# Kernel optimization log

Measured on AMD Instinct MI355X. Metric: run time of the kernel, lower is better.

The kernel has to match this reference:

```python
import jax, jax.numpy as jnp
import numpy as np

N_AGENTS = 32
N_HEADS = 8
HEAD_DIM = 32          # atten_dim // n_heads
HID = 256              # rnn_hidden_dim
ATT = 256              # atten_dim
N_ACT = 32
NEG = -1e9             # finite stand-in for -inf; exp underflows to 0 in softmax


def setup_inputs() -> dict:
    key = jax.random.key(0)
    ks = jax.random.split(key, 20)
    B, N, E = 4096, 64, 128
    w = lambda k, shape: (jax.random.normal(k, shape, jnp.float32) * 0.05)
    return {
        "inputs": jax.random.normal(ks[0], (B, N, E), jnp.float32),
        "hidden_state": jax.random.normal(ks[1], (B, N_AGENTS, HID), jnp.float32) * 0.1,
        "fc1_w": w(ks[2], (HID, E)), "fc1_b": jnp.zeros((HID,), jnp.float32),
        "q_w": w(ks[3], (ATT, HID)), "q_b": jnp.zeros((ATT,), jnp.float32),
        "k_w": w(ks[4], (ATT, HID)), "k_b": jnp.zeros((ATT,), jnp.float32),
        "v_w": w(ks[5], (ATT, HID)), "v_b": jnp.zeros((ATT,), jnp.float32),
        "w_ih": w(ks[6], (3 * HID, ATT)), "w_hh": w(ks[7], (3 * HID, HID)),
        "b_ih": jnp.zeros((3 * HID,), jnp.float32), "b_hh": jnp.zeros((3 * HID,), jnp.float32),
        "out_w": w(ks[8], (N_ACT, HID)), "out_b": jnp.zeros((N_ACT,), jnp.float32),
        "obs_mask": jax.random.randint(ks[9], (B, N, N), 0, 2).astype(bool),
        "scenario_mask": jax.random.randint(ks[10], (B, N_AGENTS), 0, 2).astype(bool),
    }


def reference(inputs, hidden_state, fc1_w, fc1_b, q_w, q_b, k_w, k_b, v_w, v_b,
              w_ih, w_hh, b_ih, b_hh, out_w, out_b, obs_mask, scenario_mask):
    B, N, _ = inputs.shape
    A, nh, e = N_AGENTS, N_HEADS, HEAD_DIM
    # fc1 + ReLU: [B, N, HID]
    x = jax.nn.relu(inputs @ fc1_w.T + fc1_b)
    # multi-head projections; queries only for the first A entities (agents)
    q = (x[:, :A] @ q_w.T + q_b).reshape(B, A, nh, e).transpose(0, 2, 1, 3)   # [B,nh,A,e]
    k = (x @ k_w.T + k_b).reshape(B, N, nh, e).transpose(0, 2, 3, 1)          # [B,nh,e,N]
    v = jax.nn.relu(x @ v_w.T + v_b).reshape(B, N, nh, e).transpose(0, 2, 1, 3)  # [B,nh,N,e]
    score = jnp.einsum('bhae,bhen->bhan', q, k) / np.float32(np.sqrt(e))      # [B,nh,A,N]
    m = obs_mask[:, :A, :][:, None, :, :]                                      # [B,1,A,N]
    score = jnp.where(m, NEG, score)
    w = jax.nn.softmax(score, axis=-1)
    # original: fully-masked rows give NaN then are zeroed; here zero all masked slots
    w = jnp.where(m, 0.0, w)
    att = jnp.einsum('bhan,bhne->bhae', w, v)                                  # [B,nh,A,e]
    att = att.transpose(0, 2, 1, 3).reshape(B * A, nh * e)                     # [B*A, ATT]
    # GRUCell step (PyTorch gate ordering: r, z, n)
    h0 = hidden_state.reshape(B * A, HID)
    gi = att @ w_ih.T + b_ih
    gh = h0 @ w_hh.T + b_hh
    ir, iz, in_ = jnp.split(gi, 3, axis=-1)
    hr, hz, hn = jnp.split(gh, 3, axis=-1)
    r = jax.nn.sigmoid(ir + hr)
    z = jax.nn.sigmoid(iz + hz)
    n = jnp.tanh(in_ + r * hn)
    h = (1.0 - z) * n + z * h0
    h = h.reshape(B, A, HID)
    am = scenario_mask[:, :, None]                                             # [B,A,1]
    h = jnp.where(am, 0.0, h)
    q_out = h @ out_w.T + out_b
    q_out = jnp.where(am, 0.0, q_out)
    return q_out, h
```

## Files before the change

### kernel.cpp

```cpp
#include <hip/hip_runtime.h>


using bfrag = __attribute__((ext_vector_type(8))) short;
using ffrag = __attribute__((ext_vector_type(4))) float;

#define MFMA(a,b,c) __builtin_amdgcn_mfma_f32_16x16x32_bf16((a),(b),(c),0,0,0)
#define SWZ(row,col,S,xm) ((row)*(S) + ((((col)&~7) ^ (((row)&(xm))<<3)) | ((col)&7)))

#define OFF_A2   0L
#define OFF_FC1  67108864L
#define OFF_QKV  67141632L
#define OFF_W6   67338240L
#define OFF_OW   67731456L
#define OFF_FLAG 67739648L
#define WS_NEED_BYTES 135479552L

__device__ inline unsigned short f2bf(float x){
  union { float f; unsigned u; } v; v.f = x;
  unsigned r = v.u + 0x7fffu + ((v.u >> 16) & 1u);
  return (unsigned short)(r >> 16);
}
__device__ inline bool getmask(const void* p, long i, int byteflag){
  return byteflag ? (((const unsigned char*)p)[i] != 0)
                  : (((const int*)p)[i] != 0);
}
__device__ inline ffrag fzero(){ ffrag z; z[0]=0.f; z[1]=0.f; z[2]=0.f; z[3]=0.f; return z; }
__device__ inline void gload16(const short* g, short* l){
  __builtin_amdgcn_global_load_lds((const __attribute__((address_space(1))) void*)g,
                                   (__attribute__((address_space(3))) void*)l, 16, 0, 0);
}
__device__ inline bfrag packbf(const float* p){
  float4 f0 = *(const float4*)p; float4 f1 = *(const float4*)(p+4);
  bfrag v;
  v[0]=(short)f2bf(f0.x); v[1]=(short)f2bf(f0.y); v[2]=(short)f2bf(f0.z); v[3]=(short)f2bf(f0.w);
  v[4]=(short)f2bf(f1.x); v[5]=(short)f2bf(f1.y); v[6]=(short)f2bf(f1.z); v[7]=(short)f2bf(f1.w);
  return v;
}

__global__ void k0_prep(const float* __restrict__ fc1, const float* __restrict__ qw,
    const float* __restrict__ kw, const float* __restrict__ vw, const float* __restrict__ wih,
    const float* __restrict__ whh, const float* __restrict__ ow,
    const void* __restrict__ obsm, short* __restrict__ ws){
  long tid = (long)blockIdx.x*blockDim.x + threadIdx.x;
  long n = (long)gridDim.x*blockDim.x;
  if (tid == 0){
    const int* mi = (const int*)obsm;
    int f = 0;
    for (int i=0;i<256;i++){ if ((unsigned)mi[i] > 1u){ f = 1; break; } }
    ((int*)(ws + OFF_FLAG))[0] = f;
  }
  for (long i=tid; i<32768; i+=n){
    int R = (int)(i>>7), c = (int)(i&127);
    int seg = R>>6, r = R&63;
    ws[OFF_FC1 + ((long)(seg*64+r)<<7) + (c ^ ((r&7)<<3))] = (short)f2bf(fc1[i]);
  }
  for (long i=tid; i<65536; i+=n){
    int R = (int)(i>>8), C = (int)(i&255);
    int cb = R>>6, r = R&63, kh = C>>7, ck = C&127;
    int cs = ck ^ ((r&7)<<3);
    ws[OFF_QKV + ((long)(((0*4+cb)*2+kh)*64 + r)<<7) + cs] = (short)f2bf(qw[i]);
    ws[OFF_QKV + ((long)(((1*4+cb)*2+kh)*64 + r)<<7) + cs] = (short)f2bf(kw[i]);
    ws[OFF_QKV + ((long)(((2*4+cb)*2+kh)*64 + r)<<7) + cs] = (short)f2bf(vw[i]);
  }
  for (long i=tid; i<196608; i+=n){
    int gate = (int)(i >> 16);
    int grow = (int)((i >> 8) & 255);
    int c = (int)(i & 255);
    int jb = grow >> 5, row = grow & 31;
    int cs = c ^ ((row&7)<<3);
    ws[OFF_W6 + ((long)((jb*6 + gate)*32 + row))*256 + cs]     = (short)f2bf(wih[i]);
    ws[OFF_W6 + ((long)((jb*6 + 3 + gate)*32 + row))*256 + cs] = (short)f2bf(whh[i]);
  }
  for (long i=tid; i<8192; i+=n) ws[OFF_OW+i] = (short)f2bf(ow[i]);
}

__global__ __launch_bounds__(512) void k1_fused(const float* __restrict__ inp,
    const short* __restrict__ fc1S, const float* __restrict__ fc1_b,
    const short* __restrict__ qkvS,
    const float* __restrict__ qb, const float* __restrict__ kb, const float* __restrict__ vb,
    const void* __restrict__ obsm, short* __restrict__ A2, const int* __restrict__ flagp){
  __shared__ __align__(16) short smem[75776];
  short* x_s  = smem;
  short* wbuf = smem + 16384;
  short* p_sb = smem + 16384;
  short* a_s  = smem + 32768;
  short* q_s  = smem + 32768;
  short* k_s  = smem + 40960;
  short* vT_s = smem + 57344;
  unsigned char* m8 = (unsigned char*)(smem + 73728);
  int t = threadIdx.x; int b = blockIdx.x;
  int lane = t&63, w = t>>6, lr = lane&15, ko = lane>>4;
  int mflag = *flagp;
  auto STG = [&](const short* src, short* dst){
    #pragma unroll
    for (int i=0;i<2;i++)
      gload16(src + (long)(i*512 + t)*8, dst + (i*512 + (t&~63))*8);
  };
  STG(fc1S, wbuf);
  #pragma unroll
  for (int i=0;i<2;i++){
    int c = t + i*512; int row = c>>4; int cc = (c&15)*8;
    *(bfrag*)(a_s + SWZ(row, cc, 128, 7)) = packbf(inp + ((long)b*64 + row)*128 + cc);
  }
  if (mflag){
    uchar4 mv = *(const uchar4*)((const unsigned char*)obsm + (long)b*4096 + t*4);
    m8[t*4]=mv.x; m8[t*4+1]=mv.y; m8[t*4+2]=mv.z; m8[t*4+3]=mv.w;
  } else {
    int4 mv = *(const int4*)((const int*)obsm + (long)b*4096 + t*4);
    m8[t*4]  =(unsigned char)(mv.x!=0); m8[t*4+1]=(unsigned char)(mv.y!=0);
    m8[t*4+2]=(unsigned char)(mv.z!=0); m8[t*4+3]=(unsigned char)(mv.w!=0);
  }
  __syncthreads();
  {
    int rg1 = w&3, ch1 = w>>2;
    bfrag a1[4];
    #pragma unroll
    for (int ks=0;ks<4;ks++)
      a1[ks] = *(const bfrag*)(a_s + SWZ(rg1*16+lr, ks*32+ko*8, 128, 7));
    for (int s=0;s<4;s++){
      STG((s<3) ? (fc1S + (s+1)*8192) : qkvS, wbuf + ((s+1)&1)*8192);
      const short* wc = wbuf + (s&1)*8192;
      ffrag acc[2]; acc[0]=fzero(); acc[1]=fzero();
      #pragma unroll
      for (int ks=0;ks<4;ks++){
        int kc = ks*32+ko*8;
        #pragma unroll
        for (int nt=0;nt<2;nt++){
          bfrag bb = *(const bfrag*)(wc + SWZ(ch1*32+nt*16+lr, kc, 128, 7));
          acc[nt] = MFMA(a1[ks], bb, acc[nt]);
        }
      }
      #pragma unroll
      for (int nt=0;nt<2;nt++){
        int colg = s*64 + ch1*32 + nt*16 + lr;
        float bias = fc1_b[colg];
        #pragma unroll
        for (int r=0;r<4;r++){
          int row = rg1*16 + ko*4 + r;
          float v = acc[nt][r] + bias; v = v>0.f?v:0.f;
          x_s[SWZ(row, colg, 256, 7)] = (short)f2bf(v);
        }
      }
      __syncthreads();
    }
  }
  {
    int rg = w&1, chs = w>>1;
    bfrag a_r[2][8];
    #pragma unroll
    for (int mt=0;mt<2;mt++)
      #pragma unroll
      for (int kk=0;kk<8;kk++)
        a_r[mt][kk] = *(const bfrag*)(x_s + SWZ(rg*32+mt*16+lr, kk*32+ko*8, 256, 7));
    ffrag acc[2];
    for (int hs=0; hs<24; hs++){
      if (hs<23) STG(qkvS + (long)(hs+1)*8192, wbuf + ((4+hs+1)&1)*8192);
      int s12 = hs>>1, kh = hs&1;
      int kind = s12>>2, cb = s12&3;
      const short* wc = wbuf + ((4+hs)&1)*8192;
      bool active = !(kind==0 && rg==1);
      if (kh==0){ acc[0]=fzero(); acc[1]=fzero(); }
      if (active){
        #pragma unroll
        for (int ks=0;ks<4;ks++){
          int kc = ks*32+ko*8;
          bfrag bb = *(const bfrag*)(wc + SWZ(chs*16+lr, kc, 128, 7));
          acc[0] = MFMA(a_r[0][kh*4+ks], bb, acc[0]);
          acc[1] = MFMA(a_r[1][kh*4+ks], bb, acc[1]);
        }
        if (kh==1){
          int colg = cb*64 + chs*16 + lr;
          float bias = (kind==0?qb:(kind==1?kb:vb))[colg];
          #pragma unroll
          for (int mt=0;mt<2;mt++){
            #pragma unroll
            for (int r=0;r<4;r++){
              int row = rg*32 + mt*16 + ko*4 + r;
              float v = acc[mt][r] + bias;
              if (kind==0){
                q_s[SWZ(row, colg, 256, 7)] = (short)f2bf(v);
              } else if (kind==1){
                k_s[SWZ(row, colg, 256, 7)] = (short)f2bf(v);
              } else {
                v = v>0.f?v:0.f;
                int hh = colg>>5, e = colg&31;
                vT_s[hh*2048 + SWZ(e, row, 64, 7)] = (short)f2bf(v);
              }
            }
          }
        }
      }
      __syncthreads();
    }
  }
  {
    const int h = w;
    short* p_s = p_sb + h*2048;
    bfrag a_q[2];
    #pragma unroll
    for (int mt=0; mt<2; mt++)
      a_q[mt] = *(const bfrag*)(q_s + SWZ(mt*16+lr, h*32+ko*8, 256, 7));
    bfrag b_k[4];
    #pragma unroll
    for (int nt=0; nt<4; nt++)
      b_k[nt] = *(const bfrag*)(k_s + SWZ(nt*16+lr, h*32+ko*8, 256, 7));
    ffrag sc[2][4];
    #pragma unroll
    for (int mt=0; mt<2; mt++)
      #pragma unroll
      for (int nt=0; nt<4; nt++) sc[mt][nt] = MFMA(a_q[mt], b_k[nt], fzero());
    const float scale = 0.17677669529663687f;
    float rsi[2][4];
    #pragma unroll
    for (int mt=0; mt<2; mt++){
      #pragma unroll
      for (int r=0; r<4; r++){
        int arow = mt*16 + ko*4 + r;
        float sv[4]; int mk[4];
        #pragma unroll
        for (int nt=0; nt<4; nt++){
          mk[nt] = m8[arow*64 + nt*16 + lr];
          sv[nt] = sc[mt][nt][r] * scale;
        }
        float mx = -3.0e38f;
        #pragma unroll
        for (int nt=0; nt<4; nt++) if (!mk[nt]) mx = fmaxf(mx, sv[nt]);
        for (int d=1; d<16; d<<=1) mx = fmaxf(mx, __shfl_xor(mx, d));
        float sum = 0.f;
        #pragma unroll
        for (int nt=0; nt<4; nt++){
          float p = mk[nt] ? 0.f : __expf(sv[nt]-mx);
          sv[nt] = p; sum += p;
        }
        for (int d=1; d<16; d<<=1) sum += __shfl_xor(sum, d);
        rsi[mt][r] = sum > 0.f ? 1.f/sum : 0.f;
        #pragma unroll
        for (int nt=0; nt<4; nt++)
          p_s[SWZ(arow, nt*16+lr, 64, 7)] = (short)f2bf(sv[nt]);
      }
    }
    ffrag o[2][2];
    #pragma unroll
    for (int mt=0;mt<2;mt++)
      #pragma unroll
      for (int nt=0;nt<2;nt++) o[mt][nt]=fzero();
    #pragma unroll
    for (int kk=0; kk<2; kk++){
      int kc = kk*32 + ko*8;
      bfrag pa0 = *(const bfrag*)(p_s + SWZ(lr,    kc, 64, 7));
      bfrag pa1 = *(const bfrag*)(p_s + SWZ(16+lr, kc, 64, 7));
      bfrag bv0 = *(const bfrag*)(vT_s + h*2048 + SWZ(lr,    kc, 64, 7));
      bfrag bv1 = *(const bfrag*)(vT_s + h*2048 + SWZ(16+lr, kc, 64, 7));
      o[0][0]=MFMA(pa0,bv0,o[0][0]); o[0][1]=MFMA(pa0,bv1,o[0][1]);
      o[1][0]=MFMA(pa1,bv0,o[1][0]); o[1][1]=MFMA(pa1,bv1,o[1][1]);
    }
    #pragma unroll
    for (int mt=0; mt<2; mt++)
      #pragma unroll
      for (int nt=0; nt<2; nt++)
        #pragma unroll
        for (int r=0; r<4; r++){
          int a = mt*16 + ko*4 + r;
          A2[((long)b*32 + a)*256 + h*32 + nt*16 + lr] = (short)f2bf(o[mt][nt][r]*rsi[mt][r]);
        }
  }
}

__global__ __launch_bounds__(512) void k3_gru(const short* __restrict__ A2,
    const float* __restrict__ h0f, const short* __restrict__ w6,
    const float* __restrict__ b_ih, const float* __restrict__ b_hh,
    const void* __restrict__ scen, float* __restrict__ hout, const int* __restrict__ flagp){
  __shared__ __align__(16) short w_s[2][16384];
  int t = threadIdx.x, bid = blockIdx.x;
  long R0 = (long)bid * 128;
  int mflag = *flagp;
  int lane = t&63, w = t>>6, lr = lane&15, ko = lane>>4;
  long rowbase = R0 + (long)w*16;
  auto STAGE = [&](int ph){
    const short* src = w6 + (long)ph*16384;
    short* dst = w_s[ph&1];
    #pragma unroll
    for (int i=0;i<4;i++)
      gload16(src + (long)(i*512 + t)*8, dst + (i*512 + (t & ~63))*8);
  };
  STAGE(0);
  const short* Ab = A2 + (rowbase + lr)*256 + ko*8;
  const float* Hb = h0f + (rowbase + lr)*256 + ko*8;
  bfrag A[16];
  #pragma unroll
  for (int ks=0; ks<8; ks++)
    A[ks] = *(const bfrag*)(Ab + ks*32);
  #pragma unroll
  for (int ks=0; ks<8; ks++)
    A[8+ks] = packbf(Hb + ks*32);
  __syncthreads();
  for (int jb=0; jb<8; jb++){
    ffrag aR[2], aZ[2], aI[2], aN[2];
    #pragma unroll
    for (int nt=0;nt<2;nt++){ aR[nt]=fzero(); aZ[nt]=fzero(); aI[nt]=fzero(); aN[nt]=fzero(); }
    #pragma unroll
    for (int p=0; p<3; p++){
      int ph = jb*3 + p;
      if (ph < 23) STAGE(ph+1);
      const short* wc = w_s[ph&1];
      #pragma unroll
      for (int ks=0; ks<8; ks++){
        int kc = ks*32 + ko*8;
        #pragma unroll
        for (int nt=0; nt<2; nt++){
          bfrag b0 = *(const bfrag*)(wc + SWZ(nt*16+lr, kc, 256, 7));
          bfrag b1 = *(const bfrag*)(wc + 8192 + SWZ(nt*16+lr, kc, 256, 7));
          if (p == 0){
            aR[nt] = MFMA(A[ks], b0, aR[nt]);
            aZ[nt] = MFMA(A[ks], b1, aZ[nt]);
          } else if (p == 1){
            aI[nt] = MFMA(A[ks], b0, aI[nt]);
            aR[nt] = MFMA(A[8+ks], b1, aR[nt]);
          } else {
            aZ[nt] = MFMA(A[8+ks], b0, aZ[nt]);
            aN[nt] = MFMA(A[8+ks], b1, aN[nt]);
          }
        }
      }
      if (p == 2){
        #pragma unroll
        for (int nt=0; nt<2; nt++){
          int j = jb*32 + nt*16 + lr;
          float bir = b_ih[j],     bhr = b_hh[j];
          float biz = b_ih[256+j], bhz = b_hh[256+j];
          float bin = b_ih[512+j], bhn = b_hh[512+j];
          #pragma unroll
          for (int rr=0; rr<4; rr++){
            long row = rowbase + ko*4 + rr;
            float rg = 1.f/(1.f + __expf(-(aR[nt][rr] + bir + bhr)));
            float zg = 1.f/(1.f + __expf(-(aZ[nt][rr] + biz + bhz)));
            float ag = aI[nt][rr] + bin + rg*(aN[nt][rr] + bhn);
            float ng = 2.f/(1.f + __expf(-2.f*ag)) - 1.f;
            float h0v = h0f[row*256 + j];
            float hv = (1.f - zg)*ng + zg*h0v;
            if (getmask(scen, row, mflag)) hv = 0.f;
            hout[row*256 + j] = hv;
          }
        }
      }
      __syncthreads();
    }
  }
}

__global__ __launch_bounds__(512) void k4_out(const float* __restrict__ hout,
    const short* __restrict__ ow, const float* __restrict__ out_b,
    const void* __restrict__ scen, float* __restrict__ qout, const int* __restrict__ flagp){
  __shared__ __align__(16) short ow_s[32*256];
  int t = threadIdx.x; long R0 = (long)blockIdx.x * 256;
  int mflag = *flagp;
  for (int i=0;i<2;i++){
    int c = t + i*512; int row = c >> 5; int cc = (c & 31)*8;
    *(bfrag*)(ow_s + SWZ(row, cc, 256, 7)) = *(const bfrag*)(ow + row*256 + cc);
  }
  __syncthreads();
  int lane = t&63, w = t>>6, lr = lane&15, ko = lane>>4;
  ffrag acc[2][2];
  #pragma unroll
  for (int a=0;a<2;a++) for (int bq=0;bq<2;bq++) acc[a][bq]=fzero();
  for (int ks=0; ks<8; ks++){
    int kc = ks*32 + ko*8;
    #pragma unroll
    for (int mi=0; mi<2; mi++){
      long row = R0 + (w*2+mi)*16 + lr;
      bfrag a = packbf(hout + row*256 + kc);
      #pragma unroll
      for (int nt=0; nt<2; nt++){
        bfrag bb = *(const bfrag*)(ow_s + SWZ(nt*16+lr, kc, 256, 7));
        acc[mi][nt] = MFMA(a, bb, acc[mi][nt]);
      }
    }
  }
  #pragma unroll
  for (int mi=0;mi<2;mi++)
    #pragma unroll
    for (int nt=0;nt<2;nt++){
      int col = nt*16 + lr;
      float ob = out_b[col];
      #pragma unroll
      for (int r=0;r<4;r++){
        long row = R0 + (w*2+mi)*16 + ko*4 + r;
        float qv = acc[mi][nt][r] + ob;
        if (getmask(scen, row, mflag)) qv = 0.f;
        qout[row*32 + col] = qv;
      }
    }
}

extern "C" void kernel_launch(void* const* d_in, const int* in_sizes, int n_in,
                              void* d_out, int out_size, void* d_ws, size_t ws_size,
                              hipStream_t stream){
  const float* inputs = (const float*)d_in[0];
  const float* hidden = (const float*)d_in[1];
  const float* fc1_w  = (const float*)d_in[2];
  const float* fc1_b  = (const float*)d_in[3];
  const float* q_w    = (const float*)d_in[4];
  const float* q_b    = (const float*)d_in[5];
  const float* k_w    = (const float*)d_in[6];
  const float* k_b    = (const float*)d_in[7];
  const float* v_w    = (const float*)d_in[8];
  const float* v_b    = (const float*)d_in[9];
  const float* w_ih   = (const float*)d_in[10];
  const float* w_hh   = (const float*)d_in[11];
  const float* b_ih   = (const float*)d_in[12];
  const float* b_hh   = (const float*)d_in[13];
  const float* out_w  = (const float*)d_in[14];
  const float* out_b  = (const float*)d_in[15];
  const void* obsm    = d_in[16];
  const void* scen    = d_in[17];
  (void)in_sizes; (void)n_in; (void)out_size;
  if ((long)ws_size < WS_NEED_BYTES) return;
  short* ws = (short*)d_ws;
  const int* flagp = (const int*)(ws + OFF_FLAG);
  float* qout = (float*)d_out;
  float* hout = qout + 4194304;
  short* A2  = ws + OFF_A2;

  hipLaunchKernelGGL(k0_prep, dim3(512), dim3(256), 0, stream,
      fc1_w, q_w, k_w, v_w, w_ih, w_hh, out_w, obsm, ws);
  hipLaunchKernelGGL(k1_fused, dim3(4096), dim3(512), 0, stream,
      inputs, ws + OFF_FC1, fc1_b, ws + OFF_QKV, q_b, k_b, v_b, obsm, A2, flagp);
  hipLaunchKernelGGL(k3_gru, dim3(1024), dim3(512), 0, stream,
      A2, hidden, ws + OFF_W6, b_ih, b_hh, scen, hout, flagp);
  hipLaunchKernelGGL(k4_out, dim3(512), dim3(512), 0, stream,
      hout, ws + OFF_OW, out_b, scen, qout, flagp);
}
```

Before: 557.2 us.

## Stage full-K QKV weight tiles and double-buffer into freed x_s

The QKV projection now streams 12 full-K (256-wide) weight tiles instead of 24 half-K tiles. The prep kernel changes the packed weight layout to match, and x_s, already copied into registers, is reused as the second staging buffer. This halves the number of block-wide barriers and staging rounds in the projection loop. The V-transpose store is also packed into 4-short vector writes. In exchange, the first QKV tile is no longer prefetched during the last fc1 step, which adds an exposed load and an extra barrier before the loop.

```diff
diff --git a/kernel.cpp b/kernel.cpp
--- a/kernel.cpp
+++ b/kernel.cpp
@@ -2,6 +2,7 @@
 
 
 using bfrag = __attribute__((ext_vector_type(8))) short;
+using s4    = __attribute__((ext_vector_type(4))) short;
 using ffrag = __attribute__((ext_vector_type(4))) float;
 
 #define MFMA(a,b,c) __builtin_amdgcn_mfma_f32_16x16x32_bf16((a),(b),(c),0,0,0)
@@ -56,11 +57,12 @@
   }
   for (long i=tid; i<65536; i+=n){
     int R = (int)(i>>8), C = (int)(i&255);
-    int cb = R>>6, r = R&63, kh = C>>7, ck = C&127;
-    int cs = ck ^ ((r&7)<<3);
-    ws[OFF_QKV + ((long)(((0*4+cb)*2+kh)*64 + r)<<7) + cs] = (short)f2bf(qw[i]);
-    ws[OFF_QKV + ((long)(((1*4+cb)*2+kh)*64 + r)<<7) + cs] = (short)f2bf(kw[i]);
-    ws[OFF_QKV + ((long)(((2*4+cb)*2+kh)*64 + r)<<7) + cs] = (short)f2bf(vw[i]);
+    int cb = R>>6, r = R&63;
+    int cs = C ^ ((r&7)<<3);
+    long base = (long)cb*16384 + (long)r*256 + cs;
+    ws[OFF_QKV + 0L*65536 + base] = (short)f2bf(qw[i]);
+    ws[OFF_QKV + 1L*65536 + base] = (short)f2bf(kw[i]);
+    ws[OFF_QKV + 2L*65536 + base] = (short)f2bf(vw[i]);
   }
   for (long i=tid; i<196608; i+=n){
     int gate = (int)(i >> 16);
@@ -80,23 +82,27 @@
     const float* __restrict__ qb, const float* __restrict__ kb, const float* __restrict__ vb,
     const void* __restrict__ obsm, short* __restrict__ A2, const int* __restrict__ flagp){
   __shared__ __align__(16) short smem[75776];
-  short* x_s  = smem;
-  short* wbuf = smem + 16384;
-  short* p_sb = smem + 16384;
-  short* a_s  = smem + 32768;
-  short* q_s  = smem + 32768;
-  short* k_s  = smem + 40960;
-  short* vT_s = smem + 57344;
+  short* x_s   = smem;
+  short* wbuf0 = smem + 16384;
+  short* a_s   = smem + 32768;
+  short* q_s   = smem + 32768;
+  short* k_s   = smem + 40960;
+  short* vT_s  = smem + 57344;
   unsigned char* m8 = (unsigned char*)(smem + 73728);
   int t = threadIdx.x; int b = blockIdx.x;
   int lane = t&63, w = t>>6, lr = lane&15, ko = lane>>4;
   int mflag = *flagp;
-  auto STG = [&](const short* src, short* dst){
+  auto STG16 = [&](const short* src, short* dst){
     #pragma unroll
     for (int i=0;i<2;i++)
       gload16(src + (long)(i*512 + t)*8, dst + (i*512 + (t&~63))*8);
   };
-  STG(fc1S, wbuf);
+  auto STG32 = [&](const short* src, short* dst){
+    #pragma unroll
+    for (int i=0;i<4;i++)
+      gload16(src + (long)(i*512 + t)*8, dst + (i*512 + (t&~63))*8);
+  };
+  STG16(fc1S, wbuf0);
   #pragma unroll
   for (int i=0;i<2;i++){
     int c = t + i*512; int row = c>>4; int cc = (c&15)*8;
@@ -118,8 +124,8 @@
     for (int ks=0;ks<4;ks++)
       a1[ks] = *(const bfrag*)(a_s + SWZ(rg1*16+lr, ks*32+ko*8, 128, 7));
     for (int s=0;s<4;s++){
-      STG((s<3) ? (fc1S + (s+1)*8192) : qkvS, wbuf + ((s+1)&1)*8192);
-      const short* wc = wbuf + (s&1)*8192;
+      if (s<3) STG16(fc1S + (s+1)*8192, wbuf0 + ((s+1)&1)*8192);
+      const short* wc = wbuf0 + (s&1)*8192;
       ffrag acc[2]; acc[0]=fzero(); acc[1]=fzero();
       #pragma unroll
       for (int ks=0;ks<4;ks++){
@@ -152,41 +158,50 @@
       #pragma unroll
       for (int kk=0;kk<8;kk++)
         a_r[mt][kk] = *(const bfrag*)(x_s + SWZ(rg*32+mt*16+lr, kk*32+ko*8, 256, 7));
-    ffrag acc[2];
-    for (int hs=0; hs<24; hs++){
-      if (hs<23) STG(qkvS + (long)(hs+1)*8192, wbuf + ((4+hs+1)&1)*8192);
-      int s12 = hs>>1, kh = hs&1;
-      int kind = s12>>2, cb = s12&3;
-      const short* wc = wbuf + ((4+hs)&1)*8192;
+    STG32(qkvS, wbuf0);
+    __syncthreads();
+    for (int s=0; s<12; s++){
+      if (s<11) STG32(qkvS + (long)(s+1)*16384, ((s+1)&1) ? x_s : wbuf0);
+      const short* wc = (s&1) ? x_s : wbuf0;
+      int kind = s>>2, cb = s&3;
       bool active = !(kind==0 && rg==1);
-      if (kh==0){ acc[0]=fzero(); acc[1]=fzero(); }
       if (active){
-        #pragma unroll
-        for (int ks=0;ks<4;ks++){
+        ffrag acc0=fzero(), acc1=fzero();
+        #pragma unroll
+        for (int ks=0;ks<8;ks++){
           int kc = ks*32+ko*8;
-          bfrag bb = *(const bfrag*)(wc + SWZ(chs*16+lr, kc, 128, 7));
-          acc[0] = MFMA(a_r[0][kh*4+ks], bb, acc[0]);
-          acc[1] = MFMA(a_r[1][kh*4+ks], bb, acc[1]);
-        }
-        if (kh==1){
-          int colg = cb*64 + chs*16 + lr;
-          float bias = (kind==0?qb:(kind==1?kb:vb))[colg];
+          bfrag bb = *(const bfrag*)(wc + SWZ(chs*16+lr, kc, 256, 7));
+          acc0 = MFMA(a_r[0][ks], bb, acc0);
+          acc1 = MFMA(a_r[1][ks], bb, acc1);
+        }
+        int colg = cb*64 + chs*16 + lr;
+        if (kind==0){
+          float bias = qb[colg];
+          #pragma unroll
+          for (int r=0;r<4;r++){
+            q_s[SWZ(ko*4+r, colg, 256, 7)]    = (short)f2bf(acc0[r] + bias);
+            q_s[SWZ(16+ko*4+r, colg, 256, 7)] = (short)f2bf(acc1[r] + bias);
+          }
+        } else if (kind==1){
+          float bias = kb[colg];
+          #pragma unroll
+          for (int r=0;r<4;r++){
+            k_s[SWZ(rg*32+ko*4+r, colg, 256, 7)]    = (short)f2bf(acc0[r] + bias);
+            k_s[SWZ(rg*32+16+ko*4+r, colg, 256, 7)] = (short)f2bf(acc1[r] + bias);
+          }
+        } else {
+          float bias = vb[colg];
+          int hh = colg>>5, e = colg&31;
           #pragma unroll
           for (int mt=0;mt<2;mt++){
+            int n0 = rg*32 + mt*16 + ko*4;
+            s4 pk;
             #pragma unroll
             for (int r=0;r<4;r++){
-              int row = rg*32 + mt*16 + ko*4 + r;
-              float v = acc[mt][r] + bias;
-              if (kind==0){
-                q_s[SWZ(row, colg, 256, 7)] = (short)f2bf(v);
-              } else if (kind==1){
-                k_s[SWZ(row, colg, 256, 7)] = (short)f2bf(v);
-              } else {
-                v = v>0.f?v:0.f;
-                int hh = colg>>5, e = colg&31;
-                vT_s[hh*2048 + SWZ(e, row, 64, 7)] = (short)f2bf(v);
-              }
+              float v = (mt?acc1[r]:acc0[r]) + bias; v = v>0.f?v:0.f;
+              pk[r] = (short)f2bf(v);
             }
+            *(s4*)(vT_s + hh*2048 + SWZ(e, n0, 64, 7)) = pk;
           }
         }
       }
@@ -195,7 +210,7 @@
   }
   {
     const int h = w;
-    short* p_s = p_sb + h*2048;
+    short* p_s = wbuf0 + h*2048;
     bfrag a_q[2];
     #pragma unroll
     for (int mt=0; mt<2; mt++)
```

New measurement: 546.0 us. 2.0% less time.
